# Optimization experiments

Hardware: AMD Instinct MI355X
Metric: run time of the kernel (lower is better)

## Reference

```python
import jax, jax.numpy as jnp
import numpy as np

N_EMBD = 1024
N_HEAD = 16
HEAD_SIZE = N_EMBD // N_HEAD  # 64
BLOCK_SIZE = 2048
HIDDEN = 2 * N_EMBD  # SwiGLU hidden
LN_EPS = 1e-5


def layernorm(x, w, b):
    m = jnp.mean(x, axis=-1, keepdims=True)
    v = jnp.mean(jnp.square(x - m), axis=-1, keepdims=True)
    return (x - m) * jax.lax.rsqrt(v + LN_EPS) * w + b


def rotate_half(x):
    # interleaved halves, exactly as the torch code: stack((-x2, x1)).reshape
    x1 = x[..., 0::2]
    x2 = x[..., 1::2]
    return jnp.stack((-x2, x1), axis=-1).reshape(x.shape)


def rope_tables(T, hd):
    inv_freq = 1.0 / (10000.0 ** (jnp.arange(0, hd, 2, dtype=jnp.float32) / hd))
    t = jnp.arange(T, dtype=jnp.float32)
    freqs = t[:, None] * inv_freq[None, :]           # [T, hd/2]
    emb = jnp.concatenate([freqs, freqs], axis=-1)   # [T, hd]
    return jnp.cos(emb), jnp.sin(emb)


def setup_inputs() -> dict:
    key = jax.random.key(0)
    ks = jax.random.split(key, 12)
    s = 0.02
    d = {
        "x": jax.random.normal(ks[0], (2, BLOCK_SIZE, N_EMBD), dtype=jnp.float32),
        "ln1_w": jnp.ones((N_EMBD,), jnp.float32),
        "ln1_b": jnp.zeros((N_EMBD,), jnp.float32),
        "ln2_w": jnp.ones((N_EMBD,), jnp.float32),
        "ln2_b": jnp.zeros((N_EMBD,), jnp.float32),
        # per-head projections, stored (H, C, hd); equivalent to x @ W.T in torch
        "Wq": jax.random.normal(ks[1], (N_HEAD, N_EMBD, HEAD_SIZE), jnp.float32) * s,
        "Wk": jax.random.normal(ks[2], (N_HEAD, N_EMBD, HEAD_SIZE), jnp.float32) * s,
        "Wv": jax.random.normal(ks[3], (N_HEAD, N_EMBD, HEAD_SIZE), jnp.float32) * s,
        "proj_w": jax.random.normal(ks[4], (N_EMBD, N_EMBD), jnp.float32) * s,
        "proj_b": jnp.zeros((N_EMBD,), jnp.float32),
        # SwiGLU MLP
        "w_w": jax.random.normal(ks[5], (N_EMBD, HIDDEN), jnp.float32) * s,
        "w_b": jnp.zeros((HIDDEN,), jnp.float32),
        "v_w": jax.random.normal(ks[6], (N_EMBD, HIDDEN), jnp.float32) * s,
        "v_b": jnp.zeros((HIDDEN,), jnp.float32),
        "p_w": jax.random.normal(ks[7], (HIDDEN, N_EMBD), jnp.float32) * s,
        "p_b": jnp.zeros((N_EMBD,), jnp.float32),
    }
    return d


def reference(x, ln1_w, ln1_b, ln2_w, ln2_b, Wq, Wk, Wv, proj_w, proj_b,
              w_w, w_b, v_w, v_b, p_w, p_b):
    B, T, C = x.shape
    # --- attention sub-block ---
    h = layernorm(x, ln1_w, ln1_b)
    q = jnp.einsum('btc,hcd->bhtd', h, Wq)
    k = jnp.einsum('btc,hcd->bhtd', h, Wk)
    v = jnp.einsum('btc,hcd->bhtd', h, Wv)
    cos, sin = rope_tables(T, HEAD_SIZE)  # [T, hd]
    cos = cos[None, None]
    sin = sin[None, None]
    q = q * cos + rotate_half(q) * sin
    k = k * cos + rotate_half(k) * sin
    scale = 1.0 / jnp.sqrt(jnp.float32(HEAD_SIZE))
    scores = jnp.einsum('bhtd,bhsd->bhts', q, k) * scale  # [B,H,T,T]
    causal = jnp.tril(jnp.ones((T, T), dtype=bool))
    scores = jnp.where(causal[None, None], scores, -jnp.inf)
    att = jax.nn.softmax(scores, axis=-1)
    o = jnp.einsum('bhts,bhsd->bhtd', att, v)
    o = o.transpose(0, 2, 1, 3).reshape(B, T, C)  # concat heads
    sa = o @ proj_w + proj_b
    x = x + sa
    # --- SwiGLU FFN sub-block ---
    h2 = layernorm(x, ln2_w, ln2_b)
    a = h2 @ w_w + w_b
    a = a * jax.nn.sigmoid(a)  # swish
    b = h2 @ v_w + v_b
    ff = (a * b) @ p_w + p_b
    return x + ff
```

## Files before the change

### kernel.cpp

```cpp
#include <hip/hip_runtime.h>
#include <math.h>

#define N_EMBD    1024
#define N_HEAD    16
#define HEAD_SIZE 64
#define T_SEQ     2048
#define BATCH     2
#define HIDDEN    2048
#define ROWS      4096

typedef __attribute__((ext_vector_type(8))) short bf16x8;
typedef __attribute__((ext_vector_type(4))) float f32x4;
typedef __attribute__((ext_vector_type(16))) float f32x16;
typedef unsigned short u16;

__device__ __forceinline__ u16 f2bf(float x) {
    union { float f; unsigned u; } v; v.f = x;
    unsigned r = v.u + 0x7fffu + ((v.u >> 16) & 1u);
    return (u16)(r >> 16);
}
__device__ __forceinline__ float bf2f(u16 h) {
    union { unsigned u; float f; } v; v.u = ((unsigned)h) << 16;
    return v.f;
}
__device__ __forceinline__ unsigned cvtpk_bf16(float lo, float hi) {
    unsigned r;
    asm volatile("v_cvt_pk_bf16_f32 %0, %1, %2" : "=v"(r) : "v"(lo), "v"(hi));
    return r;
}
__device__ __forceinline__ void gload16(const void* g, void* lds) {
    __builtin_amdgcn_global_load_lds((const __attribute__((address_space(1))) void*)g,
                                     (__attribute__((address_space(3))) void*)lds, 16, 0, 0);
}

__device__ __forceinline__ void wtrans_body(const float* s, u16* d, int ldS, int ldD,
                                            int k0, int n0, float Ts[64][65])
{
    const int tid = threadIdx.x;
    const int rr = tid >> 4, c4 = (tid & 15) * 4;
#pragma unroll
    for (int i = 0; i < 4; i++) {
        float4 v = *(const float4*)(s + (size_t)(k0 + rr + i * 16) * ldS + n0 + c4);
        Ts[rr + i * 16][c4 + 0] = v.x;
        Ts[rr + i * 16][c4 + 1] = v.y;
        Ts[rr + i * 16][c4 + 2] = v.z;
        Ts[rr + i * 16][c4 + 3] = v.w;
    }
    __syncthreads();
    const int nr = tid >> 2, kc = (tid & 3) * 16;
#pragma unroll
    for (int j = 0; j < 4; j++) {
        u16 t0 = f2bf(Ts[kc + j * 4 + 0][nr]);
        u16 t1 = f2bf(Ts[kc + j * 4 + 1][nr]);
        u16 t2 = f2bf(Ts[kc + j * 4 + 2][nr]);
        u16 t3 = f2bf(Ts[kc + j * 4 + 3][nr]);
        *(ushort4*)(d + (size_t)(n0 + nr) * ldD + k0 + kc + j * 4) = make_ushort4(t0, t1, t2, t3);
    }
}

__global__ __launch_bounds__(256) void wtrans_all(const float* __restrict__ Wq, const float* __restrict__ Wk,
                                                  const float* __restrict__ Wv, const float* __restrict__ ww,
                                                  const float* __restrict__ vv, const float* __restrict__ pw,
                                                  const float* __restrict__ ppw,
                                                  u16* __restrict__ Wqkv, u16* __restrict__ wwT,
                                                  u16* __restrict__ vvT, u16* __restrict__ pwT,
                                                  u16* __restrict__ ppT)
{
    __shared__ float Ts[64][65];
    const int b = blockIdx.x;
    const float* s; u16* d; int ldS, ldD, k0, n0;
    if (b < 768) {
        const int z = b >> 4;
        k0 = (b & 15) * 64; n0 = 0;
        const int which = z >> 4;
        s = (which == 0 ? Wq : which == 1 ? Wk : Wv) + (size_t)(z & 15) * 65536;
        d = Wqkv + (size_t)z * 65536;
        ldS = 64; ldD = 1024;
    } else if (b < 1792) {
        const int b2 = b - 768, z = b2 >> 4;
        k0 = (b2 & 15) * 64; n0 = (z & 31) * 64;
        s = (z >> 5) ? vv : ww; d = (z >> 5) ? vvT : wwT;
        ldS = 2048; ldD = 1024;
    } else if (b < 2048) {
        const int b3 = b - 1792;
        k0 = (b3 & 15) * 64; n0 = (b3 >> 4) * 64;
        s = pw; d = pwT; ldS = 1024; ldD = 1024;
    } else {
        const int b4 = b - 2048;
        k0 = (b4 & 31) * 64; n0 = (b4 >> 5) * 64;
        s = ppw; d = ppT; ldS = 1024; ldD = 2048;
    }
    wtrans_body(s, d, ldS, ldD, k0, n0, Ts);
}

__global__ __launch_bounds__(256) void ln_kernel(const float* __restrict__ x,
                                                 const float* __restrict__ w,
                                                 const float* __restrict__ b,
                                                 u16* __restrict__ out)
{
    const int row = blockIdx.x;
    const int tid = threadIdx.x;
    const float* xr = x + (size_t)row * N_EMBD;
    float4 v = *(const float4*)(xr + tid * 4);
    float s  = v.x + v.y + v.z + v.w;
    float s2 = v.x*v.x + v.y*v.y + v.z*v.z + v.w*v.w;
#pragma unroll
    for (int off = 32; off; off >>= 1) {
        s  += __shfl_xor(s, off);
        s2 += __shfl_xor(s2, off);
    }
    __shared__ float ss[4], ss2[4];
    if ((tid & 63) == 0) { ss[tid >> 6] = s; ss2[tid >> 6] = s2; }
    __syncthreads();
    s  = ss[0] + ss[1] + ss[2] + ss[3];
    s2 = ss2[0] + ss2[1] + ss2[2] + ss2[3];
    const float mean = s * (1.0f / N_EMBD);
    const float var  = s2 * (1.0f / N_EMBD) - mean * mean;
    const float rstd = rsqrtf(var + 1e-5f);
    float4 wv = *(const float4*)(w + tid * 4);
    float4 bv = *(const float4*)(b + tid * 4);
    ushort4 st = make_ushort4(f2bf((v.x - mean) * rstd * wv.x + bv.x),
                              f2bf((v.y - mean) * rstd * wv.y + bv.y),
                              f2bf((v.z - mean) * rstd * wv.z + bv.z),
                              f2bf((v.w - mean) * rstd * wv.w + bv.w));
    *(ushort4*)(out + (size_t)row * N_EMBD + tid * 4) = st;
}

__global__ __launch_bounds__(256) void rope_kernel(u16* __restrict__ q, u16* __restrict__ k)
{
    const int u = blockIdx.x * 256 + threadIdx.x;
    const int i  = u & 31;
    const int t  = (u >> 5) & (T_SEQ - 1);
    const int bh = u >> 16;
    const size_t base = ((size_t)bh * T_SEQ + t) * HEAD_SIZE + 2 * i;
    const float L = 0.28782313662425572f;
    const float QS = 0.125f * 1.44269504088896f;
    const int i0 = (2 * i) & 31, i1 = (2 * i + 1) & 31;
    float c0, s0, c1, s1;
    sincosf((float)t * __expf(-(float)i0 * L), &s0, &c0);
    sincosf((float)t * __expf(-(float)i1 * L), &s1, &c1);
    float a0 = bf2f(q[base]), a1 = bf2f(q[base + 1]);
    q[base]     = f2bf((a0 * c0 - a1 * s0) * QS);
    q[base + 1] = f2bf((a1 * c1 + a0 * s1) * QS);
    float b0 = bf2f(k[base]), b1 = bf2f(k[base + 1]);
    k[base]     = f2bf(b0 * c0 - b1 * s0);
    k[base + 1] = f2bf(b1 * c1 + b0 * s1);
}

__global__ __launch_bounds__(256) void gemm_br(const u16* __restrict__ A, const u16* __restrict__ Bt,
                                               const float* __restrict__ bias, const float* __restrict__ resid,
                                               float* __restrict__ Cf,
                                               int N, int K)
{
    __shared__ __align__(16) u16 As[2][128 * 64];
    __shared__ __align__(16) u16 Bs[2][64 * 64];
    const int tid = threadIdx.x, w = tid >> 6, l = tid & 63, l15 = l & 15, l4 = l >> 4;
    const int wm = w >> 1, wn = w & 1;
    const int n0 = blockIdx.x * 64, m0 = blockIdx.y * 128;
    f32x4 acc[4][2] = {};
    const int NT = K >> 6;

    auto stage = [&](int buf, int k0) {
#pragma unroll
        for (int c = 0; c < 4; c++) {
            const int slot = c * 256 + tid;
            const int row = slot >> 3;
            const int sw = ((slot & 7) * 16) ^ ((row & 7) << 4);
            gload16((const char*)(A + (size_t)(m0 + row) * K + k0) + sw, (char*)&As[buf][0] + slot * 16);
        }
#pragma unroll
        for (int c = 0; c < 2; c++) {
            const int slot = c * 256 + tid;
            const int row = slot >> 3;
            const int sw = ((slot & 7) * 16) ^ ((row & 7) << 4);
            gload16((const char*)(Bt + (size_t)(n0 + row) * K + k0) + sw, (char*)&Bs[buf][0] + slot * 16);
        }
    };

    stage(0, 0);
    __syncthreads();
    int cur = 0;
    for (int t = 0; t < NT; t++) {
        if (t + 1 < NT) stage(cur ^ 1, (t + 1) << 6);
#pragma unroll
        for (int ks = 0; ks < 2; ks++) {
            const int cb = ks * 64 + l4 * 16;
            bf16x8 af[4], bf[2];
#pragma unroll
            for (int mt = 0; mt < 4; mt++) {
                const int row = wm * 64 + mt * 16 + l15;
                af[mt] = *(const bf16x8*)((const char*)&As[cur][0] + row * 128 + (cb ^ ((row & 7) << 4)));
            }
#pragma unroll
            for (int u = 0; u < 2; u++) {
                const int row = wn * 32 + u * 16 + l15;
                bf[u] = *(const bf16x8*)((const char*)&Bs[cur][0] + row * 128 + (cb ^ ((row & 7) << 4)));
            }
#pragma unroll
            for (int mt = 0; mt < 4; mt++)
#pragma unroll
                for (int u = 0; u < 2; u++)
                    acc[mt][u] = __builtin_amdgcn_mfma_f32_16x16x32_bf16(af[mt], bf[u], acc[mt][u], 0, 0, 0);
        }
        __syncthreads();
        cur ^= 1;
    }
#pragma unroll
    for (int mt = 0; mt < 4; mt++) {
#pragma unroll
        for (int u = 0; u < 2; u++) {
            const int n = n0 + wn * 32 + u * 16 + l15;
            const float bi = bias[n];
#pragma unroll
            for (int r = 0; r < 4; r++) {
                const int m = m0 + wm * 64 + mt * 16 + l4 * 4 + r;
                const size_t idx = (size_t)m * N + n;
                Cf[idx] = acc[mt][u][r] + bi + resid[idx];
            }
        }
    }
}

__global__ __launch_bounds__(256, 4) void gemm_qkv(const u16* __restrict__ A, const u16* __restrict__ Bt,
                                                   u16* __restrict__ qo, u16* __restrict__ ko, u16* __restrict__ vto)
{
    __shared__ __align__(16) u16 As[2][64 * 64];
    __shared__ __align__(16) u16 Bs[2][64 * 64];
    const int tid = threadIdx.x, w = tid >> 6, l = tid & 63, l15 = l & 15, l4 = l >> 4;
    const int wm = w >> 1, wn = w & 1;
    const int n0 = blockIdx.x * 128, m0 = blockIdx.y * 128;
    const int K = N_EMBD;
    f32x4 acc[4][4] = {};
    const int NT = K >> 5;

    auto stage = [&](int buf, int k0) {
#pragma unroll
        for (int c = 0; c < 2; c++) {
            const int slot = c * 256 + tid;
            const int r2 = slot >> 3;
            const int w16u = (slot & 7) ^ (r2 & 7);
            const int grow = (w16u >> 2) * 64 + r2;
            const int kc = w16u & 3;
            gload16(A  + (size_t)(m0 + grow) * K + k0 + kc * 8, (char*)&As[buf][0] + slot * 16);
            gload16(Bt + (size_t)(n0 + grow) * K + k0 + kc * 8, (char*)&Bs[buf][0] + slot * 16);
        }
    };

    stage(0, 0);
    __syncthreads();
    int cur = 0;
    for (int t = 0; t < NT; t++) {
        if (t + 1 < NT) stage(cur ^ 1, (t + 1) << 5);
        bf16x8 af[4], bf[4];
#pragma unroll
        for (int q4 = 0; q4 < 4; q4++) {
            const int ga = wm * 64 + q4 * 16 + l15;
            const int ra = ga & 63, ha = ga >> 6;
            af[q4] = *(const bf16x8*)((const char*)&As[cur][0] + ra * 128 + (((ha << 2) | l4) ^ (ra & 7)) * 16);
            const int gb = wn * 64 + q4 * 16 + l15;
            const int rb = gb & 63, hb = gb >> 6;
            bf[q4] = *(const bf16x8*)((const char*)&Bs[cur][0] + rb * 128 + (((hb << 2) | l4) ^ (rb & 7)) * 16);
        }
#pragma unroll
        for (int mt = 0; mt < 4; mt++)
#pragma unroll
            for (int nt = 0; nt < 4; nt++)
                acc[mt][nt] = __builtin_amdgcn_mfma_f32_16x16x32_bf16(af[mt], bf[nt], acc[mt][nt], 0, 0, 0);
        __syncthreads();
        cur ^= 1;
    }
#pragma unroll
    for (int mt = 0; mt < 4; mt++) {
#pragma unroll
        for (int nt = 0; nt < 4; nt++) {
            const int n = n0 + wn * 64 + nt * 16 + l15;
            const int which = n >> 10, hd = (n >> 6) & 15, dd = n & 63;
            const int mb = m0 + wm * 64 + mt * 16 + l4 * 4;
            const int bI = mb >> 11, tq = mb & (T_SEQ - 1);
            if (which == 2) {
                ushort4 st = make_ushort4(f2bf(acc[mt][nt][0]), f2bf(acc[mt][nt][1]),
                                          f2bf(acc[mt][nt][2]), f2bf(acc[mt][nt][3]));
                *(ushort4*)(vto + ((size_t)(bI * N_HEAD + hd) * HEAD_SIZE + dd) * T_SEQ + tq) = st;
            } else {
                u16* dst = (which == 0) ? qo : ko;
#pragma unroll
                for (int r = 0; r < 4; r++)
                    dst[((size_t)(bI * N_HEAD + hd) * T_SEQ + tq + r) * HEAD_SIZE + dd] = f2bf(acc[mt][nt][r]);
            }
        }
    }
}

__global__ __launch_bounds__(256, 4) void gemm_glu(const u16* __restrict__ A, const u16* __restrict__ Bw,
                                                   const u16* __restrict__ Bv,
                                                   const float* __restrict__ wb, const float* __restrict__ vb,
                                                   u16* __restrict__ G)
{
    __shared__ __align__(16) u16 As[2][64 * 64];
    __shared__ __align__(16) u16 Bws[2][32 * 64];
    __shared__ __align__(16) u16 Bvs[2][32 * 64];
    const int tid = threadIdx.x, w = tid >> 6, l = tid & 63, l15 = l & 15, l4 = l >> 4;
    const int wm = w >> 1, wn = w & 1;
    const int n0 = blockIdx.x * 64, m0 = blockIdx.y * 128;
    const int K = N_EMBD;
    f32x4 accA[4][2] = {};
    f32x4 accB[4][2] = {};
    const int NT = K >> 5;

    auto stage = [&](int buf, int k0) {
#pragma unroll
        for (int c = 0; c < 2; c++) {
            const int slot = c * 256 + tid;
            const int r2 = slot >> 3;
            const int w16u = (slot & 7) ^ (r2 & 7);
            const int grow = (w16u >> 2) * 64 + r2;
            const int kc = w16u & 3;
            gload16(A + (size_t)(m0 + grow) * K + k0 + kc * 8, (char*)&As[buf][0] + slot * 16);
        }
        {
            const int slot = tid;
            const int r2 = slot >> 3;
            const int w16u = (slot & 7) ^ (r2 & 7);
            const int grow = (w16u >> 2) * 32 + r2;
            const int kc = w16u & 3;
            gload16(Bw + (size_t)(n0 + grow) * K + k0 + kc * 8, (char*)&Bws[buf][0] + slot * 16);
            gload16(Bv + (size_t)(n0 + grow) * K + k0 + kc * 8, (char*)&Bvs[buf][0] + slot * 16);
        }
    };

    stage(0, 0);
    __syncthreads();
    int cur = 0;
    for (int t = 0; t < NT; t++) {
        if (t + 1 < NT) stage(cur ^ 1, (t + 1) << 5);
        bf16x8 af[4], bwf[2], bvf[2];
#pragma unroll
        for (int q4 = 0; q4 < 4; q4++) {
            const int ga = wm * 64 + q4 * 16 + l15;
            const int ra = ga & 63, ha = ga >> 6;
            af[q4] = *(const bf16x8*)((const char*)&As[cur][0] + ra * 128 + (((ha << 2) | l4) ^ (ra & 7)) * 16);
        }
#pragma unroll
        for (int u = 0; u < 2; u++) {
            const int gb = wn * 32 + u * 16 + l15;
            const int rb = gb & 31, hb = gb >> 5;
            const int off = rb * 128 + (((hb << 2) | l4) ^ (rb & 7)) * 16;
            bwf[u] = *(const bf16x8*)((const char*)&Bws[cur][0] + off);
            bvf[u] = *(const bf16x8*)((const char*)&Bvs[cur][0] + off);
        }
#pragma unroll
        for (int mt = 0; mt < 4; mt++)
#pragma unroll
            for (int u = 0; u < 2; u++) {
                accA[mt][u] = __builtin_amdgcn_mfma_f32_16x16x32_bf16(af[mt], bwf[u], accA[mt][u], 0, 0, 0);
                accB[mt][u] = __builtin_amdgcn_mfma_f32_16x16x32_bf16(af[mt], bvf[u], accB[mt][u], 0, 0, 0);
            }
        __syncthreads();
        cur ^= 1;
    }
#pragma unroll
    for (int mt = 0; mt < 4; mt++) {
#pragma unroll
        for (int u = 0; u < 2; u++) {
            const int n = n0 + wn * 32 + u * 16 + l15;
            const float wbi = wb[n], vbi = vb[n];
#pragma unroll
            for (int r = 0; r < 4; r++) {
                const int m = m0 + wm * 64 + mt * 16 + l4 * 4 + r;
                const float a  = accA[mt][u][r] + wbi;
                const float bb = accB[mt][u][r] + vbi;
                G[(size_t)m * HIDDEN + n] = f2bf(a / (1.f + __expf(-a)) * bb);
            }
        }
    }
}

__global__ __launch_bounds__(256, 4) void attn_mfma(const u16* __restrict__ q, const u16* __restrict__ k,
                                                    const u16* __restrict__ vt, u16* __restrict__ o)
{
    __shared__ __align__(16) u16 Kb[2][64 * 64];
    __shared__ __align__(16) u16 Vb[2][64 * 64];
    __shared__ float ml[2][32];
    const int tid = threadIdx.x, l = tid & 63, l31 = l & 31, hh2 = (l >> 5) & 1;
    const int wid  = tid >> 6;
    const int qsub = wid >> 1;
    const int par  = wid & 1;
    const int bh  = blockIdx.x;
    const int qtb = (int)gridDim.y - 1 - (int)blockIdx.y;
    const int qt  = qtb * 2 + qsub;
    const int qw0 = qt * 32;
    const int nc  = qtb + 1;
    const u16* qb  = q  + (size_t)bh * T_SEQ * HEAD_SIZE;
    const u16* kbg = k  + (size_t)bh * T_SEQ * HEAD_SIZE;
    const u16* vbg = vt + (size_t)bh * HEAD_SIZE * T_SEQ;

    bf16x8 qf[4];
    {
        const u16* qr = qb + (size_t)(qw0 + l31) * HEAD_SIZE + hh2 * 8;
#pragma unroll
        for (int kk = 0; kk < 4; kk++) qf[kk] = *(const bf16x8*)(qr + kk * 16);
    }
    bf16x8 onesf;
#pragma unroll
    for (int e = 0; e < 8; e++) onesf[e] = (short)0x3F80;

    f32x16 oacc0 = {}, oacc1 = {}, lacc = {};
    const float M0 = 20.f;

    auto stage = [&](int buf, int s0) {
#pragma unroll
        for (int c = 0; c < 2; c++) {
            const int slot = c * 256 + tid;
            const int row = slot >> 3;
            const int sw = ((slot & 7) * 16) ^ ((row & 7) << 4);
            gload16((const char*)(kbg + (size_t)(s0 + row) * HEAD_SIZE) + sw, (char*)&Kb[buf][0] + slot * 16);
        }
#pragma unroll
        for (int c = 0; c < 2; c++) {
            const int slot = c * 256 + tid;
            const int row = slot >> 3;
            const int sw = ((slot & 7) * 16) ^ ((row & 7) << 4);
            gload16((const char*)(vbg + (size_t)row * T_SEQ + s0) + sw, (char*)&Vb[buf][0] + slot * 16);
        }
    };

    stage(0, 0);
    __syncthreads();
    int cur = 0;

    for (int j = 0; j < nc; j++) {
        if (j + 1 < nc) stage(cur ^ 1, (j + 1) * 64);

        const int hc = 2 * j + par;
        if (hc <= qt) {
            f32x16 sa;
#pragma unroll
            for (int reg = 0; reg < 16; reg++) sa[reg] = -M0;
            const int row = par * 32 + l31;
            const int swz = (row & 7) << 4;
#pragma unroll
            for (int kk = 0; kk < 4; kk++) {
                const bf16x8 kf = *(const bf16x8*)((const char*)&Kb[cur][0] + row * 128 + ((kk * 32 + hh2 * 16) ^ swz));
                sa = __builtin_amdgcn_mfma_f32_32x32x16_bf16(kf, qf[kk], sa, 0, 0, 0);
            }
            if (hc == qt) {
#pragma unroll
                for (int reg = 0; reg < 16; reg++) {
                    const int R = (reg & 3) + 8 * (reg >> 2) + 4 * hh2;
                    if (R > l31) sa[reg] = -1e30f;
                }
            }
#pragma unroll
            for (int reg = 0; reg < 16; reg++) sa[reg] = exp2f(sa[reg]);

            unsigned pk[8];
#pragma unroll
            for (int jj = 0; jj < 8; jj++) pk[jj] = cvtpk_bf16(sa[2 * jj], sa[2 * jj + 1]);

#pragma unroll
            for (int st = 0; st < 2; st++) {
                const int b = st * 4;
                union { unsigned u[4]; bf16x8 v; } r;
                const unsigned s0w = (unsigned)__shfl_xor((int)pk[b + 0], 32);
                const unsigned s1w = (unsigned)__shfl_xor((int)pk[b + 1], 32);
                const unsigned s2w = (unsigned)__shfl_xor((int)pk[b + 2], 32);
                const unsigned s3w = (unsigned)__shfl_xor((int)pk[b + 3], 32);
                r.u[0] = hh2 ? s2w : pk[b + 0];
                r.u[1] = hh2 ? s3w : pk[b + 1];
                r.u[2] = hh2 ? pk[b + 2] : s0w;
                r.u[3] = hh2 ? pk[b + 3] : s1w;
                lacc = __builtin_amdgcn_mfma_f32_32x32x16_bf16(onesf, r.v, lacc, 0, 0, 0);
#pragma unroll
                for (int dt = 0; dt < 2; dt++) {
                    const int vrow = dt * 32 + l31;
                    const int vswz = (vrow & 7) << 4;
                    const int vcol = (par * 64 + st * 32 + hh2 * 16) ^ vswz;
                    const bf16x8 vf = *(const bf16x8*)((const char*)&Vb[cur][0] + vrow * 128 + vcol);
                    if (dt == 0) oacc0 = __builtin_amdgcn_mfma_f32_32x32x16_bf16(vf, r.v, oacc0, 0, 0, 0);
                    else         oacc1 = __builtin_amdgcn_mfma_f32_32x32x16_bf16(vf, r.v, oacc1, 0, 0, 0);
                }
            }
        }
        __syncthreads();
        cur ^= 1;
    }

    float* obuf = (float*)&Kb[0][0] + (size_t)qsub * 2048;
    if (par == 1) {
#pragma unroll
        for (int reg = 0; reg < 16; reg++) {
            const int R = (reg & 3) + 8 * (reg >> 2) + 4 * hh2;
            obuf[R * 32 + l31] = oacc0[reg];
            obuf[(32 + R) * 32 + l31] = oacc1[reg];
        }
        if (hh2 == 0) ml[qsub][l31] = lacc[0];
    }
    __syncthreads();
    if (par == 0) {
        const float inv = 1.f / (lacc[0] + ml[qsub][l31]);
        const int bI = bh >> 4, hd = bh & 15;
        u16* ob = o + ((size_t)(bI * T_SEQ + qw0 + l31)) * N_EMBD + hd * HEAD_SIZE;
#pragma unroll
        for (int g = 0; g < 4; g++) {
            const int d0a = g * 8 + hh2 * 4;
            float v0[4], v1[4];
#pragma unroll
            for (int r = 0; r < 4; r++) {
                const int R = d0a + r;
                v0[r] = (oacc0[4 * g + r] + obuf[R * 32 + l31]) * inv;
                v1[r] = (oacc1[4 * g + r] + obuf[(32 + R) * 32 + l31]) * inv;
            }
            *(ushort4*)(ob + d0a)      = make_ushort4(f2bf(v0[0]), f2bf(v0[1]), f2bf(v0[2]), f2bf(v0[3]));
            *(ushort4*)(ob + 32 + d0a) = make_ushort4(f2bf(v1[0]), f2bf(v1[1]), f2bf(v1[2]), f2bf(v1[3]));
        }
    }
}

extern "C" void kernel_launch(void* const* d_in, const int* in_sizes, int n_in,
                              void* d_out, int out_size, void* d_ws, size_t ws_size,
                              hipStream_t stream)
{
    (void)in_sizes; (void)n_in; (void)out_size; (void)ws_size;
    const float* x      = (const float*)d_in[0];
    const float* ln1_w  = (const float*)d_in[1];
    const float* ln1_b  = (const float*)d_in[2];
    const float* ln2_w  = (const float*)d_in[3];
    const float* ln2_b  = (const float*)d_in[4];
    const float* Wq     = (const float*)d_in[5];
    const float* Wk     = (const float*)d_in[6];
    const float* Wv     = (const float*)d_in[7];
    const float* proj_w = (const float*)d_in[8];
    const float* proj_b = (const float*)d_in[9];
    const float* w_w    = (const float*)d_in[10];
    const float* w_b    = (const float*)d_in[11];
    const float* v_w    = (const float*)d_in[12];
    const float* v_b    = (const float*)d_in[13];
    const float* p_w    = (const float*)d_in[14];
    const float* p_b    = (const float*)d_in[15];
    float* out = (float*)d_out;

    char* W = (char*)d_ws;
    u16*   Wqkv = (u16*)(W + 0);
    u16*   pwT  = (u16*)(W + 6291456);
    u16*   wwT  = (u16*)(W + 8388608);
    u16*   vvT  = (u16*)(W + 12582912);
    u16*   ppT  = (u16*)(W + 16777216);
    u16*   h    = (u16*)(W + 20971520);
    u16*   qB   = (u16*)(W + 29360128);
    u16*   kB   = (u16*)(W + 37748736);
    u16*   vtB  = (u16*)(W + 46137344);
    u16*   oB   = (u16*)(W + 54525952);
    float* x1   = (float*)(W + 62914560);
    u16*   ga   = qB;

    wtrans_all<<<2560, 256, 0, stream>>>(Wq, Wk, Wv, w_w, v_w, proj_w, p_w,
                                         Wqkv, wwT, vvT, pwT, ppT);

    ln_kernel<<<ROWS, 256, 0, stream>>>(x, ln1_w, ln1_b, h);
    gemm_qkv<<<dim3(24, 32), 256, 0, stream>>>(h, Wqkv, qB, kB, vtB);
    rope_kernel<<<(BATCH * N_HEAD * T_SEQ * 32) / 256, 256, 0, stream>>>(qB, kB);
    attn_mfma<<<dim3(BATCH * N_HEAD, T_SEQ / 64), 256, 0, stream>>>(qB, kB, vtB, oB);
    gemm_br<<<dim3(16, 32), 256, 0, stream>>>(oB, pwT, proj_b, x, x1, N_EMBD, N_EMBD);
    ln_kernel<<<ROWS, 256, 0, stream>>>(x1, ln2_w, ln2_b, h);
    gemm_glu<<<dim3(32, 32), 256, 0, stream>>>(h, wwT, vvT, w_b, v_b, ga);
    gemm_br<<<dim3(16, 32), 256, 0, stream>>>(ga, ppT, p_b, x1, out, N_EMBD, HIDDEN);
}
```

Before: 200.3 us.

## Single-buffer attention K/V tiles, compute row sums with VALU, raise occupancy

The attention kernel drops double-buffered K/V shared memory in favour of a single buffer that is loaded synchronously each iteration. It replaces the ones-matrix MFMA used for the softmax denominator with a scalar per-lane sum plus a cross-half shuffle, and raises the launch bound to 8 blocks per SM. The aim is to cut LDS use and registers (no lacc accumulator) so more waves can hide latency, at the cost of losing the prefetch overlap between global loads and compute. Row sums now come from fp32 values rather than bf16-rounded ones, which changes numerics slightly.

```diff
diff --git a/kernel.cpp b/kernel.cpp
--- a/kernel.cpp
+++ b/kernel.cpp
@@ -375,11 +375,11 @@
     }
 }
 
-__global__ __launch_bounds__(256, 4) void attn_mfma(const u16* __restrict__ q, const u16* __restrict__ k,
+__global__ __launch_bounds__(256, 8) void attn_mfma(const u16* __restrict__ q, const u16* __restrict__ k,
                                                     const u16* __restrict__ vt, u16* __restrict__ o)
 {
-    __shared__ __align__(16) u16 Kb[2][64 * 64];
-    __shared__ __align__(16) u16 Vb[2][64 * 64];
+    __shared__ __align__(16) u16 Kb[64 * 64];
+    __shared__ __align__(16) u16 Vb[64 * 64];
     __shared__ float ml[2][32];
     const int tid = threadIdx.x, l = tid & 63, l31 = l & 31, hh2 = (l >> 5) & 1;
     const int wid  = tid >> 6;
@@ -400,36 +400,32 @@
 #pragma unroll
         for (int kk = 0; kk < 4; kk++) qf[kk] = *(const bf16x8*)(qr + kk * 16);
     }
-    bf16x8 onesf;
-#pragma unroll
-    for (int e = 0; e < 8; e++) onesf[e] = (short)0x3F80;
-
-    f32x16 oacc0 = {}, oacc1 = {}, lacc = {};
+
+    f32x16 oacc0 = {}, oacc1 = {};
+    float lrow = 0.f;
     const float M0 = 20.f;
 
-    auto stage = [&](int buf, int s0) {
+    auto stage = [&](int s0) {
 #pragma unroll
         for (int c = 0; c < 2; c++) {
             const int slot = c * 256 + tid;
             const int row = slot >> 3;
             const int sw = ((slot & 7) * 16) ^ ((row & 7) << 4);
-            gload16((const char*)(kbg + (size_t)(s0 + row) * HEAD_SIZE) + sw, (char*)&Kb[buf][0] + slot * 16);
+            gload16((const char*)(kbg + (size_t)(s0 + row) * HEAD_SIZE) + sw, (char*)&Kb[0] + slot * 16);
         }
 #pragma unroll
         for (int c = 0; c < 2; c++) {
             const int slot = c * 256 + tid;
             const int row = slot >> 3;
             const int sw = ((slot & 7) * 16) ^ ((row & 7) << 4);
-            gload16((const char*)(vbg + (size_t)row * T_SEQ + s0) + sw, (char*)&Vb[buf][0] + slot * 16);
+            gload16((const char*)(vbg + (size_t)row * T_SEQ + s0) + sw, (char*)&Vb[0] + slot * 16);
         }
     };
 
-    stage(0, 0);
-    __syncthreads();
-    int cur = 0;
-
     for (int j = 0; j < nc; j++) {
-        if (j + 1 < nc) stage(cur ^ 1, (j + 1) * 64);
+        if (j) __syncthreads();
+        stage(j * 64);
+        __syncthreads();
 
         const int hc = 2 * j + par;
         if (hc <= qt) {
@@ -440,7 +436,7 @@
             const int swz = (row & 7) << 4;
 #pragma unroll
             for (int kk = 0; kk < 4; kk++) {
-                const bf16x8 kf = *(const bf16x8*)((const char*)&Kb[cur][0] + row * 128 + ((kk * 32 + hh2 * 16) ^ swz));
+                const bf16x8 kf = *(const bf16x8*)((const char*)&Kb[0] + row * 128 + ((kk * 32 + hh2 * 16) ^ swz));
                 sa = __builtin_amdgcn_mfma_f32_32x32x16_bf16(kf, qf[kk], sa, 0, 0, 0);
             }
             if (hc == qt) {
@@ -450,8 +446,15 @@
                     if (R > l31) sa[reg] = -1e30f;
                 }
             }
-#pragma unroll
-            for (int reg = 0; reg < 16; reg++) sa[reg] = exp2f(sa[reg]);
+            float ls = 0.f;
+#pragma unroll
+            for (int reg = 0; reg < 16; reg++) {
+                const float pv = exp2f(sa[reg]);
+                sa[reg] = pv;
+                ls += pv;
+            }
+            ls += __shfl_xor(ls, 32);
+            lrow += ls;
 
             unsigned pk[8];
 #pragma unroll
@@ -469,23 +472,21 @@
                 r.u[1] = hh2 ? s3w : pk[b + 1];
                 r.u[2] = hh2 ? pk[b + 2] : s0w;
                 r.u[3] = hh2 ? pk[b + 3] : s1w;
-                lacc = __builtin_amdgcn_mfma_f32_32x32x16_bf16(onesf, r.v, lacc, 0, 0, 0);
 #pragma unroll
                 for (int dt = 0; dt < 2; dt++) {
                     const int vrow = dt * 32 + l31;
                     const int vswz = (vrow & 7) << 4;
                     const int vcol = (par * 64 + st * 32 + hh2 * 16) ^ vswz;
-                    const bf16x8 vf = *(const bf16x8*)((const char*)&Vb[cur][0] + vrow * 128 + vcol);
+                    const bf16x8 vf = *(const bf16x8*)((const char*)&Vb[0] + vrow * 128 + vcol);
                     if (dt == 0) oacc0 = __builtin_amdgcn_mfma_f32_32x32x16_bf16(vf, r.v, oacc0, 0, 0, 0);
                     else         oacc1 = __builtin_amdgcn_mfma_f32_32x32x16_bf16(vf, r.v, oacc1, 0, 0, 0);
                 }
             }
         }
-        __syncthreads();
-        cur ^= 1;
-    }
-
-    float* obuf = (float*)&Kb[0][0] + (size_t)qsub * 2048;
+    }
+
+    __syncthreads();
+    float* obuf = qsub ? (float*)&Vb[0] : (float*)&Kb[0];
     if (par == 1) {
 #pragma unroll
         for (int reg = 0; reg < 16; reg++) {
@@ -493,11 +494,11 @@
             obuf[R * 32 + l31] = oacc0[reg];
             obuf[(32 + R) * 32 + l31] = oacc1[reg];
         }
-        if (hh2 == 0) ml[qsub][l31] = lacc[0];
+        if (hh2 == 0) ml[qsub][l31] = lrow;
     }
     __syncthreads();
     if (par == 0) {
-        const float inv = 1.f / (lacc[0] + ml[qsub][l31]);
+        const float inv = 1.f / (lrow + ml[qsub][l31]);
         const int bI = bh >> 4, hd = bh & 15;
         u16* ob = o + ((size_t)(bI * T_SEQ + qw0 + l31)) * N_EMBD + hd * HEAD_SIZE;
 #pragma unroll
```

Result: slower. 361.4 us (+80.4%).
